# Kernel optimization log

Measured on AMD Instinct MI355X. Metric: run time of the kernel, lower is better.

The kernel has to match this reference:

```python
import jax, jax.numpy as jnp
import numpy as np

N, T, S, H, HC, LMH = 100, 2, 6, 64, 64, 128  # zones, timesteps, state, actor/critic GRU hidden, localized hidden
MAX_ACTION = 3.0
NB = (S + 1) * 5  # 35: neighbor-concat feature size


def setup_inputs() -> dict:
    key = jax.random.key(0)
    ks = iter(jax.random.split(key, 40))
    def rn(shape, s=0.05):
        return jax.random.normal(next(ks), shape, dtype=jnp.float32) * s
    B = 2048
    return {
        "x": jax.random.normal(next(ks), (B, T, N, S), dtype=jnp.float32),
        # 100 independent SubActor parameter sets, stacked along leading unit axis
        "a_Wih": rn((N, 3 * H, S)), "a_Whh": rn((N, 3 * H, H)),
        "a_bih": rn((N, 3 * H)), "a_bhh": rn((N, 3 * H)),
        "a_W1": rn((N, H, H)), "a_b1": rn((N, H)),
        "a_W2": rn((N, H, H)), "a_b2": rn((N, H)),
        "a_W3": rn((N, 1, H)), "a_b3": rn((N, 1)),
        # LocalizedModule 99 (only index 99 survives the buggy critic loop)
        "lm_W1": rn((LMH, NB)), "lm_b1": rn((LMH,)),
        "lm_W2": rn((LMH, LMH)), "lm_b2": rn((LMH,)),
        "lm_W3": rn((1, LMH)), "lm_b3": rn((1,)),
        # SubCritic 99
        "sc_Wih": rn((3 * HC, NB)), "sc_Whh": rn((3 * HC, HC)),
        "sc_bih": rn((3 * HC,)), "sc_bhh": rn((3 * HC,)),
        "sc_W1": rn((HC, HC)), "sc_b1": rn((HC,)),
        "sc_W2": rn((HC, HC)), "sc_b2": rn((HC,)),
        "sc_W3": rn((1, HC)), "sc_b3": rn((1,)),
    }


def _gru_cell(gx, gh, h):
    # PyTorch GRU gate order: r, z, n
    xr, xz, xn = jnp.split(gx, 3, axis=-1)
    hr, hz, hn = jnp.split(gh, 3, axis=-1)
    r = jax.nn.sigmoid(xr + hr)
    z = jax.nn.sigmoid(xz + hz)
    n = jnp.tanh(xn + r * hn)
    return (1.0 - z) * n + z * h


def _forward(x, a_Wih, a_Whh, a_bih, a_bhh, a_W1, a_b1, a_W2, a_b2, a_W3, a_b3,
             lm_W1, lm_b1, lm_W2, lm_b2, lm_W3, lm_b3,
             sc_Wih, sc_Whh, sc_bih, sc_bhh, sc_W1, sc_b1, sc_W2, sc_b2, sc_W3, sc_b3):
    B = x.shape[0]
    # ---- ActorNetwork: 100 independent GRU+MLP units, batched over unit axis n ----
    gx = jnp.einsum('btns,ngs->btng', x, a_Wih) + a_bih  # [B,T,N,3H]
    def astep(h, gx_t):
        gh = jnp.einsum('bnh,ngh->bng', h, a_Whh) + a_bhh
        h2 = _gru_cell(gx_t, gh, h)
        return h2, h2
    h0 = jnp.zeros((B, N, H), x.dtype)
    _, hs = jax.lax.scan(astep, h0, jnp.moveaxis(gx, 1, 0))
    hseq = jnp.moveaxis(hs, 0, 1)  # [B,T,N,H]
    a = jax.nn.relu(hseq)
    a = jax.nn.relu(jnp.einsum('btnh,nkh->btnk', a, a_W1) + a_b1)
    a = jax.nn.relu(jnp.einsum('btnh,nkh->btnk', a, a_W2) + a_b2)
    a = MAX_ACTION * (jax.nn.sigmoid(jnp.einsum('btnh,nkh->btnk', a, a_W3) + a_b3) - 0.5)  # [B,T,N,1]
    # torch.stack over units -> (N,B,T,1), then .view(-1,T,N): subactor-major flat reinterpretation
    p = jnp.transpose(a[..., 0], (2, 0, 1)).reshape(B, T, N)
    xc = jnp.concatenate([x, p[..., None]], axis=-1)  # [B,T,N,S+1]
    # ---- CriticNetwork: f/q lists are reset inside the loop, so only i=99 contributes ----
    # neighbors of 99: (99, 89, 100->zeros, 109->zeros, 98)
    z7 = jnp.zeros_like(xc[:, :, 99])
    xi = jnp.concatenate([xc[:, :, 99], xc[:, :, 89], z7, z7, xc[:, :, 98]], axis=-1)  # [B,T,35]
    # LocalizedModule 99 on last timestep
    f = jax.nn.relu(xi[:, -1] @ lm_W1.T + lm_b1)
    f = jax.nn.relu(f @ lm_W2.T + lm_b2)
    f = f @ lm_W3.T + lm_b3  # [B,1]
    # SubCritic 99: GRU then per-timestep MLP; only last timestep is returned,
    # and the MLP is per-timestep, so applying it to the last hidden state is exact.
    cgx = xi @ sc_Wih.T + sc_bih  # [B,T,3HC]
    def cstep(h, gx_t):
        gh = h @ sc_Whh.T + sc_bhh
        h2 = _gru_cell(gx_t, gh, h)
        return h2, h2
    h_last, _ = jax.lax.scan(cstep, jnp.zeros((B, HC), x.dtype), jnp.moveaxis(cgx, 1, 0))
    c = jax.nn.relu(h_last)
    c = jax.nn.relu(c @ sc_W1.T + sc_b1)
    c = jax.nn.relu(c @ sc_W2.T + sc_b2)
    q = c @ sc_W3.T + sc_b3  # [B,1]
    q_total = jnp.sum(f + q, axis=1)  # [B]
    return p[:, -1], q_total.reshape(-1, 1)


def reference(x, a_Wih, a_Whh, a_bih, a_bhh, a_W1, a_b1, a_W2, a_b2, a_W3, a_b3,
              lm_W1, lm_b1, lm_W2, lm_b2, lm_W3, lm_b3,
              sc_Wih, sc_Whh, sc_bih, sc_bhh, sc_W1, sc_b1, sc_W2, sc_b2, sc_W3, sc_b3):
    return _forward(x, a_Wih, a_Whh, a_bih, a_bhh, a_W1, a_b1, a_W2, a_b2, a_W3, a_b3,
                    lm_W1, lm_b1, lm_W2, lm_b2, lm_W3, lm_b3,
                    sc_Wih, sc_Whh, sc_bih, sc_bhh, sc_W1, sc_b1, sc_W2, sc_b2, sc_W3, sc_b3)
```

## Files before the change

kernel.cpp:

```cpp
#include <hip/hip_runtime.h>
#include <hip/hip_bf16.h>

typedef __attribute__((ext_vector_type(8))) short short8;
typedef __attribute__((ext_vector_type(4))) float f32x4;

#define SLAB 44032
#define WS_W_OFF 1638400
#define WS_CW_OFF (WS_W_OFF + 100 * SLAB)
#define E_SLAB 1100800
#define E_CW   48064

#define OFF_X 44032
#define OFF_H 48128
#define OFF_A 64512
#define LDS_TOTAL 80896

__device__ __forceinline__ unsigned pkbf(float a, float b) {
    __hip_bfloat162 h = __float22bfloat162_rn(make_float2(a, b));
    return *reinterpret_cast<unsigned*>(&h);
}
__device__ __forceinline__ float sigf(float x) {
    return __builtin_amdgcn_rcpf(1.f + __builtin_amdgcn_exp2f(-1.4426950408889634f * x));
}
__device__ __forceinline__ float tanhfast(float y) {
    return 1.f - 2.f * __builtin_amdgcn_rcpf(1.f + __builtin_amdgcn_exp2f(2.8853900817779268f * y));
}
__device__ __forceinline__ void g2l16(const void* g, void* l) {
    __builtin_amdgcn_global_load_lds(
        (const __attribute__((address_space(1))) void*)g,
        (__attribute__((address_space(3))) void*)l, 16, 0, 0);
}

__global__ __launch_bounds__(256)
void convert_kernel(const float* __restrict__ Wih, const float* __restrict__ Whh,
                    const float* __restrict__ W1, const float* __restrict__ W2,
                    const float* __restrict__ scWih, const float* __restrict__ scWhh,
                    const float* __restrict__ scW1, const float* __restrict__ scW2,
                    const float* __restrict__ lmW1, const float* __restrict__ lmW2,
                    char* __restrict__ slab, float* __restrict__ cw)
{
    int idx = blockIdx.x * 256 + threadIdx.x;
    if (idx < E_SLAB) {
        int n = idx / 11008;
        int i = idx - n * 11008;
        char* zs = slab + (size_t)n * SLAB;
        if (i < 768) {
            int row = i >> 2, j = i & 3;
            const float* g = Wih + n * 1152 + row * 6;
            float a = (2 * j < 6) ? g[2 * j] : 0.f;
            float b = (2 * j + 1 < 6) ? g[2 * j + 1] : 0.f;
            *(unsigned*)(zs + row * 16 + j * 4) = pkbf(a, b);
        } else if (i < 6912) {
            int k = i - 768, row = k >> 5, j = k & 31;
            float2 v = *(const float2*)(Whh + n * 12288 + row * 64 + j * 2);
            *(unsigned*)(zs + 3072 + row * 128 + ((j * 4) ^ ((row & 7) << 4))) = pkbf(v.x, v.y);
        } else if (i < 8960) {
            int k = i - 6912, row = k >> 5, j = k & 31;
            float2 v = *(const float2*)(W1 + n * 4096 + row * 64 + j * 2);
            *(unsigned*)(zs + 27648 + row * 128 + ((j * 4) ^ ((row & 7) << 4))) = pkbf(v.x, v.y);
        } else {
            int k = i - 8960, row = k >> 5, j = k & 31;
            float2 v = *(const float2*)(W2 + n * 4096 + row * 64 + j * 2);
            *(unsigned*)(zs + 35840 + row * 128 + ((j * 4) ^ ((row & 7) << 4))) = pkbf(v.x, v.y);
        }
        return;
    }
    int i = idx - E_SLAB;
    if (i >= E_CW) return;
    float v;
    if (i < 6720)        { int c = i / 192,          j = i - c * 192;          v = scWih[j * 35 + c]; }
    else if (i < 19008)  { int k = (i - 6720) / 192, j = (i - 6720) - k * 192; v = scWhh[j * 64 + k]; }
    else if (i < 23104)  { int k = (i - 19008) / 64, j = (i - 19008) - k * 64; v = scW1[j * 64 + k]; }
    else if (i < 27200)  { int k = (i - 23104) / 64, j = (i - 23104) - k * 64; v = scW2[j * 64 + k]; }
    else if (i < 31680)  { int c = (i - 27200) / 128, j = (i - 27200) - c * 128; v = lmW1[j * 35 + c]; }
    else                 { int k = (i - 31680) / 128, j = (i - 31680) - k * 128; v = lmW2[j * 128 + k]; }
    cw[i] = v;
}

__global__ __launch_bounds__(256, 2)
void actor_kernel(const float* __restrict__ x, const char* __restrict__ slab,
                  const float* __restrict__ bih, const float* __restrict__ bhh,
                  const float* __restrict__ b1, const float* __restrict__ b2,
                  const float* __restrict__ W3, const float* __restrict__ b3,
                  float* __restrict__ p_flat)
{
    extern __shared__ char sm[];
    const int tid   = threadIdx.x;
    const int n     = blockIdx.x >> 4;
    const int chunk = blockIdx.x & 15;
    const int w     = tid >> 6;
    const int l     = tid & 63;
    const int bcol  = l & 15;
    const int grp   = l >> 4;
    const int a7    = bcol & 7;
    const int ch0   = grp * 4;

    {
        const char* gz = slab + (size_t)n * SLAB;
        for (int i = w; i < 43; i += 4)
            g2l16(gz + i * 1024 + l * 16, sm + i * 1024);
        int t = tid >> 7, b = tid & 127;
        const float* xr = x + (size_t)(chunk * 128 + b) * 1200 + t * 600 + n * 6;
        uint4 pk;
        pk.x = pkbf(xr[0], xr[1]);
        pk.y = pkbf(xr[2], xr[3]);
        pk.z = pkbf(xr[4], xr[5]);
        pk.w = 0u;
        *(uint4*)(sm + OFF_X + (t * 128 + b) * 16) = pk;
    }
    __syncthreads();

    const int gsz = (grp ^ a7) << 4;
    const char* wihp = sm + bcol * 16;
    const char* whhA = sm + 3072  + bcol * 128 + gsz;
    const char* whhB = sm + 3072  + bcol * 128 + (gsz ^ 64);
    const char* w1A  = sm + 27648 + bcol * 128 + gsz;
    const char* w1B  = sm + 27648 + bcol * 128 + (gsz ^ 64);
    const char* w2A  = sm + 35840 + bcol * 128 + gsz;
    const char* w2B  = sm + 35840 + bcol * 128 + (gsz ^ 64);
    char* hTile = sm + OFF_H + w * 4096;
    char* aTile = sm + OFF_A + w * 4096;
    const int wgr = (grp & 1) * 8;
    const int g1v = grp >> 1;

    const float* bihz = bih + n * 192;
    const float* bhhz = bhh + n * 192;
    f32x4 bRi[4], bZi[4], bXNi[4], bHNi[4];
#pragma unroll
    for (int mt = 0; mt < 4; ++mt) {
        const int ch = mt * 16 + ch0;
        bRi[mt]  = *(const f32x4*)&bihz[ch]      + *(const f32x4*)&bhhz[ch];
        bZi[mt]  = *(const f32x4*)&bihz[64 + ch] + *(const f32x4*)&bhhz[64 + ch];
        bXNi[mt] = *(const f32x4*)&bihz[128 + ch];
        bHNi[mt] = *(const f32x4*)&bhhz[128 + ch];
    }
    const float b3v = b3[n];
    const short8 zfrag = {0, 0, 0, 0, 0, 0, 0, 0};

    f32x4 hp[2][4];
#pragma unroll
    for (int nt = 0; nt < 2; ++nt)
#pragma unroll
        for (int mt = 0; mt < 4; ++mt) hp[nt][mt] = (f32x4){0.f, 0.f, 0.f, 0.f};

    for (int t = 0; t < 2; ++t) {
        short8 bxv[2] = {zfrag, zfrag};
        if (grp == 0) {
            bxv[0] = *(const short8*)(sm + OFF_X + (t * 128 + w * 32 + bcol) * 16);
            bxv[1] = *(const short8*)(sm + OFF_X + (t * 128 + w * 32 + 16 + bcol) * 16);
        }
        short8 bh0v[2], bh1v[2];
        if (t == 1) {
#pragma unroll
            for (int nt = 0; nt < 2; ++nt) {
                bh0v[nt] = *(const short8*)(hTile + (nt * 16 + bcol) * 128 + gsz);
                bh1v[nt] = *(const short8*)(hTile + (nt * 16 + bcol) * 128 + (gsz ^ 64));
            }
        }
#pragma unroll
        for (int mt = 0; mt < 4; ++mt) {
            f32x4 aR[2], aZ[2], aXN[2], aHN[2];
#pragma unroll
            for (int nt = 0; nt < 2; ++nt) {
                aR[nt] = bRi[mt]; aZ[nt] = bZi[mt]; aXN[nt] = bXNi[mt]; aHN[nt] = bHNi[mt];
            }
            short8 wr = zfrag, wzg = zfrag, wn = zfrag;
            if (grp == 0) {
                wr  = *(const short8*)(wihp + (0 + mt) * 256);
                wzg = *(const short8*)(wihp + (4 + mt) * 256);
                wn  = *(const short8*)(wihp + (8 + mt) * 256);
            }
#pragma unroll
            for (int nt = 0; nt < 2; ++nt) {
                aR[nt]  = __builtin_amdgcn_mfma_f32_16x16x32_bf16(wr,  bxv[nt], aR[nt],  0, 0, 0);
                aZ[nt]  = __builtin_amdgcn_mfma_f32_16x16x32_bf16(wzg, bxv[nt], aZ[nt],  0, 0, 0);
                aXN[nt] = __builtin_amdgcn_mfma_f32_16x16x32_bf16(wn,  bxv[nt], aXN[nt], 0, 0, 0);
            }
            if (t == 1) {
                short8 r0 = *(const short8*)(whhA + (0 + mt) * 2048);
                short8 r1 = *(const short8*)(whhB + (0 + mt) * 2048);
                short8 z0 = *(const short8*)(whhA + (4 + mt) * 2048);
                short8 z1 = *(const short8*)(whhB + (4 + mt) * 2048);
                short8 n0 = *(const short8*)(whhA + (8 + mt) * 2048);
                short8 n1 = *(const short8*)(whhB + (8 + mt) * 2048);
#pragma unroll
                for (int nt = 0; nt < 2; ++nt) {
                    aR[nt]  = __builtin_amdgcn_mfma_f32_16x16x32_bf16(r0, bh0v[nt], aR[nt],  0, 0, 0);
                    aR[nt]  = __builtin_amdgcn_mfma_f32_16x16x32_bf16(r1, bh1v[nt], aR[nt],  0, 0, 0);
                    aZ[nt]  = __builtin_amdgcn_mfma_f32_16x16x32_bf16(z0, bh0v[nt], aZ[nt],  0, 0, 0);
                    aZ[nt]  = __builtin_amdgcn_mfma_f32_16x16x32_bf16(z1, bh1v[nt], aZ[nt],  0, 0, 0);
                    aHN[nt] = __builtin_amdgcn_mfma_f32_16x16x32_bf16(n0, bh0v[nt], aHN[nt], 0, 0, 0);
                    aHN[nt] = __builtin_amdgcn_mfma_f32_16x16x32_bf16(n1, bh1v[nt], aHN[nt], 0, 0, 0);
                }
            }
#pragma unroll
            for (int nt = 0; nt < 2; ++nt) {
                f32x4 h2;
#pragma unroll
                for (int r = 0; r < 4; ++r) {
                    float rg = sigf(aR[nt][r]);
                    float zg = sigf(aZ[nt][r]);
                    float nn = tanhfast(aXN[nt][r] + rg * aHN[nt][r]);
                    h2[r] = nn + zg * (hp[nt][mt][r] - nn);
                }
                hp[nt][mt] = h2;
                char* wmt = hTile + nt * 2048 + bcol * 128 + wgr + (((2 * mt + g1v) ^ a7) << 4);
                if (t == 0) {
                    uint2 ph; ph.x = pkbf(h2[0], h2[1]); ph.y = pkbf(h2[2], h2[3]);
                    *(uint2*)wmt = ph;
                }
                uint2 pa;
                pa.x = pkbf(fmaxf(h2[0], 0.f), fmaxf(h2[1], 0.f));
                pa.y = pkbf(fmaxf(h2[2], 0.f), fmaxf(h2[3], 0.f));
                *(uint2*)(wmt + 16384) = pa;
            }
        }
        {
            short8 ba0[2], ba1[2];
#pragma unroll
            for (int nt = 0; nt < 2; ++nt) {
                ba0[nt] = *(const short8*)(aTile + (nt * 16 + bcol) * 128 + gsz);
                ba1[nt] = *(const short8*)(aTile + (nt * 16 + bcol) * 128 + (gsz ^ 64));
            }
#pragma unroll
            for (int mt = 0; mt < 4; ++mt) {
                short8 wa  = *(const short8*)(w1A + mt * 2048);
                short8 wbv = *(const short8*)(w1B + mt * 2048);
                f32x4 bmv = *(const f32x4*)&b1[n * 64 + mt * 16 + ch0];
#pragma unroll
                for (int nt = 0; nt < 2; ++nt) {
                    f32x4 m1 = bmv;
                    m1 = __builtin_amdgcn_mfma_f32_16x16x32_bf16(wa,  ba0[nt], m1, 0, 0, 0);
                    m1 = __builtin_amdgcn_mfma_f32_16x16x32_bf16(wbv, ba1[nt], m1, 0, 0, 0);
                    uint2 pm;
                    pm.x = pkbf(fmaxf(m1[0], 0.f), fmaxf(m1[1], 0.f));
                    pm.y = pkbf(fmaxf(m1[2], 0.f), fmaxf(m1[3], 0.f));
                    *(uint2*)(aTile + nt * 2048 + bcol * 128 + wgr + (((2 * mt + g1v) ^ a7) << 4)) = pm;
                }
            }
        }
        {
            short8 bm0[2], bm1[2];
#pragma unroll
            for (int nt = 0; nt < 2; ++nt) {
                bm0[nt] = *(const short8*)(aTile + (nt * 16 + bcol) * 128 + gsz);
                bm1[nt] = *(const short8*)(aTile + (nt * 16 + bcol) * 128 + (gsz ^ 64));
            }
            float part[2] = {0.f, 0.f};
#pragma unroll
            for (int mt = 0; mt < 4; ++mt) {
                short8 wa  = *(const short8*)(w2A + mt * 2048);
                short8 wbv = *(const short8*)(w2B + mt * 2048);
                f32x4 bmv = *(const f32x4*)&b2[n * 64 + mt * 16 + ch0];
                f32x4 w3v = *(const f32x4*)&W3[n * 64 + mt * 16 + ch0];
#pragma unroll
                for (int nt = 0; nt < 2; ++nt) {
                    f32x4 m2 = bmv;
                    m2 = __builtin_amdgcn_mfma_f32_16x16x32_bf16(wa,  bm0[nt], m2, 0, 0, 0);
                    m2 = __builtin_amdgcn_mfma_f32_16x16x32_bf16(wbv, bm1[nt], m2, 0, 0, 0);
#pragma unroll
                    for (int r = 0; r < 4; ++r)
                        part[nt] += w3v[r] * fmaxf(m2[r], 0.f);
                }
            }
#pragma unroll
            for (int nt = 0; nt < 2; ++nt) {
                part[nt] += __shfl_xor(part[nt], 16, 64);
                part[nt] += __shfl_xor(part[nt], 32, 64);
            }
            if (l < 16) {
#pragma unroll
                for (int nt = 0; nt < 2; ++nt) {
                    int bg = chunk * 128 + w * 32 + nt * 16 + bcol;
                    float val = 3.f * (sigf(part[nt] + b3v) - 0.5f);
                    p_flat[n * 4096 + bg * 2 + t] = val;
                }
            }
        }
    }
}

__global__ __launch_bounds__(256, 2)
void critic_kernel(const float* __restrict__ x, const float* __restrict__ p_flat,
                   const float* __restrict__ cw,
                   const float* __restrict__ lmb1, const float* __restrict__ lmb2,
                   const float* __restrict__ lmW3, const float* __restrict__ lmb3,
                   const float* __restrict__ scbih, const float* __restrict__ scbhh,
                   const float* __restrict__ scb1, const float* __restrict__ scb2,
                   const float* __restrict__ scW3, const float* __restrict__ scb3,
                   float* __restrict__ out)
{
    const float* tWih = cw;
    const float* tWhh = cw + 6720;
    const float* tW1  = cw + 19008;
    const float* tW2  = cw + 23104;
    const float* tlm1 = cw + 27200;
    const float* tlm2 = cw + 31680;

    __shared__ float sxi[4][72];
    __shared__ float shh[4][68];
    __shared__ float sab[4][68];
    __shared__ float sc1[4][68];
    __shared__ float sf1[4][132];

    const int tid = threadIdx.x;
    const int wid = tid >> 6;
    const int lane = tid & 63;
    const int b = blockIdx.x * 4 + wid;

    for (int idx = lane; idx < 72; idx += 64) {
        int t = idx / 36, c = idx - t * 36;
        float v = 0.f;
        if (c < 35) {
            int g = c / 7, e = c - g * 7;
            int z = (g == 0) ? 99 : (g == 1) ? 89 : (g == 4) ? 98 : -1;
            if (z >= 0)
                v = (e < 6) ? x[((size_t)b * 2 + t) * 600 + z * 6 + e]
                            : p_flat[b * 200 + t * 100 + z];
        }
        sxi[wid][idx] = v;
    }
    __syncthreads();

    float cg00 = scbih[lane], cg01 = scbih[lane + 64], cg02 = scbih[lane + 128];
    float cg10 = cg00, cg11 = cg01, cg12 = cg02;
#pragma unroll 5
    for (int c = 0; c < 35; ++c) {
        float w0 = tWih[c * 192 + lane];
        float w1 = tWih[c * 192 + 64 + lane];
        float w2 = tWih[c * 192 + 128 + lane];
        float x0 = sxi[wid][c], x1 = sxi[wid][36 + c];
        cg00 += w0 * x0; cg01 += w1 * x0; cg02 += w2 * x0;
        cg10 += w0 * x1; cg11 += w1 * x1; cg12 += w2 * x1;
    }
    const float bhr = scbhh[lane], bhz = scbhh[lane + 64], bhn = scbhh[lane + 128];
    float r  = 1.f / (1.f + expf(-(cg00 + bhr)));
    float zg = 1.f / (1.f + expf(-(cg01 + bhz)));
    float nn = tanhf(cg02 + r * bhn);
    float hj = (1.f - zg) * nn;
    shh[wid][lane] = hj;
    __syncthreads();
    float ghr = bhr, ghz = bhz, ghn = bhn;
#pragma unroll 8
    for (int k = 0; k < 64; ++k) {
        float hk = shh[wid][k];
        ghr += tWhh[k * 192 + lane] * hk;
        ghz += tWhh[k * 192 + 64 + lane] * hk;
        ghn += tWhh[k * 192 + 128 + lane] * hk;
    }
    r  = 1.f / (1.f + expf(-(cg10 + ghr)));
    zg = 1.f / (1.f + expf(-(cg11 + ghz)));
    nn = tanhf(cg12 + r * ghn);
    hj = (1.f - zg) * nn + zg * hj;
    sab[wid][lane] = fmaxf(hj, 0.f);
    __syncthreads();
    float acc = scb1[lane];
#pragma unroll 8
    for (int k = 0; k < 64; ++k)
        acc += tW1[k * 64 + lane] * sab[wid][k];
    sc1[wid][lane] = fmaxf(acc, 0.f);
    __syncthreads();
    float acc2 = scb2[lane];
#pragma unroll 8
    for (int k = 0; k < 64; ++k)
        acc2 += tW2[k * 64 + lane] * sc1[wid][k];
    float qpart = scW3[lane] * fmaxf(acc2, 0.f);
    float f1a = lmb1[lane], f1c = lmb1[lane + 64];
#pragma unroll 5
    for (int c = 0; c < 35; ++c) {
        float xv = sxi[wid][36 + c];
        f1a += tlm1[c * 128 + lane] * xv;
        f1c += tlm1[c * 128 + 64 + lane] * xv;
    }
    sf1[wid][lane] = fmaxf(f1a, 0.f);
    sf1[wid][lane + 64] = fmaxf(f1c, 0.f);
    __syncthreads();
    float f2a = lmb2[lane], f2c = lmb2[lane + 64];
#pragma unroll 8
    for (int k = 0; k < 128; ++k) {
        float fv = sf1[wid][k];
        f2a += tlm2[k * 128 + lane] * fv;
        f2c += tlm2[k * 128 + 64 + lane] * fv;
    }
    float fpart = lmW3[lane] * fmaxf(f2a, 0.f) + lmW3[lane + 64] * fmaxf(f2c, 0.f);

    float tot = qpart + fpart;
    for (int m = 32; m > 0; m >>= 1) tot += __shfl_xor(tot, m, 64);
    if (lane == 0) out[204800 + b] = tot + scb3[0] + lmb3[0];

    for (int l2 = lane; l2 < 100; l2 += 64)
        out[b * 100 + l2] = p_flat[b * 200 + 100 + l2];
}

extern "C" void kernel_launch(void* const* d_in, const int* in_sizes, int n_in,
                              void* d_out, int out_size, void* d_ws, size_t ws_size,
                              hipStream_t stream) {
    const float* x     = (const float*)d_in[0];
    const float* aWih  = (const float*)d_in[1];
    const float* aWhh  = (const float*)d_in[2];
    const float* abih  = (const float*)d_in[3];
    const float* abhh  = (const float*)d_in[4];
    const float* aW1   = (const float*)d_in[5];
    const float* ab1   = (const float*)d_in[6];
    const float* aW2   = (const float*)d_in[7];
    const float* ab2   = (const float*)d_in[8];
    const float* aW3   = (const float*)d_in[9];
    const float* ab3   = (const float*)d_in[10];
    const float* lmW1  = (const float*)d_in[11];
    const float* lmb1  = (const float*)d_in[12];
    const float* lmW2  = (const float*)d_in[13];
    const float* lmb2  = (const float*)d_in[14];
    const float* lmW3  = (const float*)d_in[15];
    const float* lmb3  = (const float*)d_in[16];
    const float* scWih = (const float*)d_in[17];
    const float* scWhh = (const float*)d_in[18];
    const float* scbih = (const float*)d_in[19];
    const float* scbhh = (const float*)d_in[20];
    const float* scW1  = (const float*)d_in[21];
    const float* scb1  = (const float*)d_in[22];
    const float* scW2  = (const float*)d_in[23];
    const float* scb2  = (const float*)d_in[24];
    const float* scW3  = (const float*)d_in[25];
    const float* scb3  = (const float*)d_in[26];
    float* out = (float*)d_out;
    float* p_flat = (float*)d_ws;
    char* slab = (char*)d_ws + WS_W_OFF;
    float* cw  = (float*)((char*)d_ws + WS_CW_OFF);

    hipFuncSetAttribute((const void*)actor_kernel,
                        hipFuncAttributeMaxDynamicSharedMemorySize, LDS_TOTAL);

    convert_kernel<<<dim3((E_SLAB + E_CW + 255) / 256), 256, 0, stream>>>(
        aWih, aWhh, aW1, aW2, scWih, scWhh, scW1, scW2, lmW1, lmW2, slab, cw);

    actor_kernel<<<dim3(1600), 256, LDS_TOTAL, stream>>>(
        x, slab, abih, abhh, ab1, ab2, aW3, ab3, p_flat);

    critic_kernel<<<dim3(512), 256, 0, stream>>>(
        x, p_flat, cw, lmb1, lmb2, lmW3, lmb3,
        scbih, scbhh, scb1, scb2, scW3, scb3, out);
}
```

Measured before the change: 78.20 us.

## Process two batch sub-chunks per actor block to amortize weight slab loads

The actor grid is halved so each block handles 256 batch rows in two sequential sub-chunks. The per-unit weight slab is staged into LDS once and reused for both, halving total global-to-LDS weight traffic. The second sub-chunk's inputs are prefetched into registers up front. MFMA sections are wrapped in s_setprio raises, and the per-warp x tile layout is reworked. Fewer blocks (800 on a large GPU) may reduce parallelism and latency hiding.

```diff
diff --git a/kernel.cpp b/kernel.cpp
--- a/kernel.cpp
+++ b/kernel.cpp
@@ -86,27 +86,37 @@
 {
     extern __shared__ char sm[];
     const int tid   = threadIdx.x;
-    const int n     = blockIdx.x >> 4;
-    const int chunk = blockIdx.x & 15;
+    const int n     = blockIdx.x >> 3;
+    const int bigc  = blockIdx.x & 7;
     const int w     = tid >> 6;
     const int l     = tid & 63;
     const int bcol  = l & 15;
     const int grp   = l >> 4;
     const int a7    = bcol & 7;
     const int ch0   = grp * 4;
-
+    char* uXw = sm + OFF_X + w * 1024;
+
+    float f1x0, f1x1, f1x2, f1x3, f1x4, f1x5;
     {
         const char* gz = slab + (size_t)n * SLAB;
         for (int i = w; i < 43; i += 4)
             g2l16(gz + i * 1024 + l * 16, sm + i * 1024);
-        int t = tid >> 7, b = tid & 127;
-        const float* xr = x + (size_t)(chunk * 128 + b) * 1200 + t * 600 + n * 6;
+        int tt = l >> 5, bb = l & 31;
+        const float* xr0 = x + (size_t)(bigc * 256 + w * 32 + bb) * 1200 + tt * 600 + n * 6;
+        const float* xr1 = xr0 + 128 * 1200;
+        float2 a0 = *(const float2*)xr0;
+        float2 a1 = *(const float2*)(xr0 + 2);
+        float2 a2 = *(const float2*)(xr0 + 4);
+        float2 c0 = *(const float2*)xr1;
+        float2 c1 = *(const float2*)(xr1 + 2);
+        float2 c2 = *(const float2*)(xr1 + 4);
+        f1x0 = c0.x; f1x1 = c0.y; f1x2 = c1.x; f1x3 = c1.y; f1x4 = c2.x; f1x5 = c2.y;
         uint4 pk;
-        pk.x = pkbf(xr[0], xr[1]);
-        pk.y = pkbf(xr[2], xr[3]);
-        pk.z = pkbf(xr[4], xr[5]);
+        pk.x = pkbf(a0.x, a0.y);
+        pk.y = pkbf(a1.x, a1.y);
+        pk.z = pkbf(a2.x, a2.y);
         pk.w = 0u;
-        *(uint4*)(sm + OFF_X + (t * 128 + b) * 16) = pk;
+        *(uint4*)(uXw + (tt * 32 + bb) * 16) = pk;
     }
     __syncthreads();
 
@@ -137,143 +147,169 @@
     const float b3v = b3[n];
     const short8 zfrag = {0, 0, 0, 0, 0, 0, 0, 0};
 
-    f32x4 hp[2][4];
-#pragma unroll
-    for (int nt = 0; nt < 2; ++nt)
-#pragma unroll
-        for (int mt = 0; mt < 4; ++mt) hp[nt][mt] = (f32x4){0.f, 0.f, 0.f, 0.f};
-
-    for (int t = 0; t < 2; ++t) {
-        short8 bxv[2] = {zfrag, zfrag};
-        if (grp == 0) {
-            bxv[0] = *(const short8*)(sm + OFF_X + (t * 128 + w * 32 + bcol) * 16);
-            bxv[1] = *(const short8*)(sm + OFF_X + (t * 128 + w * 32 + 16 + bcol) * 16);
+    for (int sc = 0; sc < 2; ++sc) {
+        if (sc == 1) {
+            int tt = l >> 5, bb = l & 31;
+            uint4 pk;
+            pk.x = pkbf(f1x0, f1x1);
+            pk.y = pkbf(f1x2, f1x3);
+            pk.z = pkbf(f1x4, f1x5);
+            pk.w = 0u;
+            *(uint4*)(uXw + (tt * 32 + bb) * 16) = pk;
         }
-        short8 bh0v[2], bh1v[2];
-        if (t == 1) {
-#pragma unroll
-            for (int nt = 0; nt < 2; ++nt) {
-                bh0v[nt] = *(const short8*)(hTile + (nt * 16 + bcol) * 128 + gsz);
-                bh1v[nt] = *(const short8*)(hTile + (nt * 16 + bcol) * 128 + (gsz ^ 64));
+        f32x4 hp[2][4];
+#pragma unroll
+        for (int nt = 0; nt < 2; ++nt)
+#pragma unroll
+            for (int mt = 0; mt < 4; ++mt) hp[nt][mt] = (f32x4){0.f, 0.f, 0.f, 0.f};
+
+        for (int t = 0; t < 2; ++t) {
+            short8 bxv[2] = {zfrag, zfrag};
+            if (grp == 0) {
+                bxv[0] = *(const short8*)(uXw + (t * 32 + bcol) * 16);
+                bxv[1] = *(const short8*)(uXw + (t * 32 + 16 + bcol) * 16);
             }
-        }
-#pragma unroll
-        for (int mt = 0; mt < 4; ++mt) {
-            f32x4 aR[2], aZ[2], aXN[2], aHN[2];
-#pragma unroll
-            for (int nt = 0; nt < 2; ++nt) {
-                aR[nt] = bRi[mt]; aZ[nt] = bZi[mt]; aXN[nt] = bXNi[mt]; aHN[nt] = bHNi[mt];
+            short8 bh0v[2], bh1v[2];
+            if (t == 1) {
+#pragma unroll
+                for (int nt = 0; nt < 2; ++nt) {
+                    bh0v[nt] = *(const short8*)(hTile + (nt * 16 + bcol) * 128 + gsz);
+                    bh1v[nt] = *(const short8*)(hTile + (nt * 16 + bcol) * 128 + (gsz ^ 64));
+                }
             }
-            short8 wr = zfrag, wzg = zfrag, wn = zfrag;
-            if (grp == 0) {
-                wr  = *(const short8*)(wihp + (0 + mt) * 256);
-                wzg = *(const short8*)(wihp + (4 + mt) * 256);
-                wn  = *(const short8*)(wihp + (8 + mt) * 256);
+#pragma unroll
+            for (int mt = 0; mt < 4; ++mt) {
+                f32x4 aR[2], aZ[2], aXN[2], aHN[2];
+#pragma unroll
+                for (int nt = 0; nt < 2; ++nt) {
+                    aR[nt] = bRi[mt]; aZ[nt] = bZi[mt]; aXN[nt] = bXNi[mt]; aHN[nt] = bHNi[mt];
+                }
+                short8 wr = zfrag, wzg = zfrag, wn = zfrag;
+                if (grp == 0) {
+                    wr  = *(const short8*)(wihp + (0 + mt) * 256);
+                    wzg = *(const short8*)(wihp + (4 + mt) * 256);
+                    wn  = *(const short8*)(wihp + (8 + mt) * 256);
+                }
+                __builtin_amdgcn_s_setprio(1);
+#pragma unroll
+                for (int nt = 0; nt < 2; ++nt) {
+                    aR[nt]  = __builtin_amdgcn_mfma_f32_16x16x32_bf16(wr,  bxv[nt], aR[nt],  0, 0, 0);
+                    aZ[nt]  = __builtin_amdgcn_mfma_f32_16x16x32_bf16(wzg, bxv[nt], aZ[nt],  0, 0, 0);
+                    aXN[nt] = __builtin_amdgcn_mfma_f32_16x16x32_bf16(wn,  bxv[nt], aXN[nt], 0, 0, 0);
+                }
+                if (t == 1) {
+                    short8 r0 = *(const short8*)(whhA + (0 + mt) * 2048);
+                    short8 r1 = *(const short8*)(whhB + (0 + mt) * 2048);
+                    short8 z0 = *(const short8*)(whhA + (4 + mt) * 2048);
+                    short8 z1 = *(const short8*)(whhB + (4 + mt) * 2048);
+                    short8 n0 = *(const short8*)(whhA + (8 + mt) * 2048);
+                    short8 n1 = *(const short8*)(whhB + (8 + mt) * 2048);
+#pragma unroll
+                    for (int nt = 0; nt < 2; ++nt) {
+                        aR[nt]  = __builtin_amdgcn_mfma_f32_16x16x32_bf16(r0, bh0v[nt], aR[nt],  0, 0, 0);
+                        aR[nt]  = __builtin_amdgcn_mfma_f32_16x16x32_bf16(r1, bh1v[nt], aR[nt],  0, 0, 0);
+                        aZ[nt]  = __builtin_amdgcn_mfma_f32_16x16x32_bf16(z0, bh0v[nt], aZ[nt],  0, 0, 0);
+                        aZ[nt]  = __builtin_amdgcn_mfma_f32_16x16x32_bf16(z1, bh1v[nt], aZ[nt],  0, 0, 0);
+                        aHN[nt] = __builtin_amdgcn_mfma_f32_16x16x32_bf16(n0, bh0v[nt], aHN[nt], 0, 0, 0);
+                        aHN[nt] = __builtin_amdgcn_mfma_f32_16x16x32_bf16(n1, bh1v[nt], aHN[nt], 0, 0, 0);
+                    }
+                }
+                __builtin_amdgcn_s_setprio(0);
+#pragma unroll
+                for (int nt = 0; nt < 2; ++nt) {
+                    f32x4 h2;
+#pragma unroll
+                    for (int r = 0; r < 4; ++r) {
+                        float rg = sigf(aR[nt][r]);
+                        float zg = sigf(aZ[nt][r]);
+                        float nn = tanhfast(aXN[nt][r] + rg * aHN[nt][r]);
+                        h2[r] = nn + zg * (hp[nt][mt][r] - nn);
+                    }
+                    hp[nt][mt] = h2;
+                    char* wmt = hTile + nt * 2048 + bcol * 128 + wgr + (((2 * mt + g1v) ^ a7) << 4);
+                    if (t == 0) {
+                        uint2 ph; ph.x = pkbf(h2[0], h2[1]); ph.y = pkbf(h2[2], h2[3]);
+                        *(uint2*)wmt = ph;
+                    }
+                    uint2 pa;
+                    pa.x = pkbf(fmaxf(h2[0], 0.f), fmaxf(h2[1], 0.f));
+                    pa.y = pkbf(fmaxf(h2[2], 0.f), fmaxf(h2[3], 0.f));
+                    *(uint2*)(wmt + 16384) = pa;
+                }
             }
-#pragma unroll
-            for (int nt = 0; nt < 2; ++nt) {
-                aR[nt]  = __builtin_amdgcn_mfma_f32_16x16x32_bf16(wr,  bxv[nt], aR[nt],  0, 0, 0);
-                aZ[nt]  = __builtin_amdgcn_mfma_f32_16x16x32_bf16(wzg, bxv[nt], aZ[nt],  0, 0, 0);
-                aXN[nt] = __builtin_amdgcn_mfma_f32_16x16x32_bf16(wn,  bxv[nt], aXN[nt], 0, 0, 0);
+            {
+                short8 ba0[2], ba1[2];
+#pragma unroll
+                for (int nt = 0; nt < 2; ++nt) {
+                    ba0[nt] = *(const short8*)(aTile + (nt * 16 + bcol) * 128 + gsz);
+                    ba1[nt] = *(const short8*)(aTile + (nt * 16 + bcol) * 128 + (gsz ^ 64));
+                }
+#pragma unroll
+                for (int mt = 0; mt < 4; ++mt) {
+                    short8 wa  = *(const short8*)(w1A + mt * 2048);
+                    short8 wbv = *(const short8*)(w1B + mt * 2048);
+                    f32x4 bmv = *(const f32x4*)&b1[n * 64 + mt * 16 + ch0];
+                    __builtin_amdgcn_s_setprio(1);
+                    f32x4 m1o[2];
+#pragma unroll
+                    for (int nt = 0; nt < 2; ++nt) {
+                        f32x4 m1 = bmv;
+                        m1 = __builtin_amdgcn_mfma_f32_16x16x32_bf16(wa,  ba0[nt], m1, 0, 0, 0);
+                        m1 = __builtin_amdgcn_mfma_f32_16x16x32_bf16(wbv, ba1[nt], m1, 0, 0, 0);
+                        m1o[nt] = m1;
+                    }
+                    __builtin_amdgcn_s_setprio(0);
+#pragma unroll
+                    for (int nt = 0; nt < 2; ++nt) {
+                        uint2 pm;
+                        pm.x = pkbf(fmaxf(m1o[nt][0], 0.f), fmaxf(m1o[nt][1], 0.f));
+                        pm.y = pkbf(fmaxf(m1o[nt][2], 0.f), fmaxf(m1o[nt][3], 0.f));
+                        *(uint2*)(aTile + nt * 2048 + bcol * 128 + wgr + (((2 * mt + g1v) ^ a7) << 4)) = pm;
+                    }
+                }
             }
-            if (t == 1) {
-                short8 r0 = *(const short8*)(whhA + (0 + mt) * 2048);
-                short8 r1 = *(const short8*)(whhB + (0 + mt) * 2048);
-                short8 z0 = *(const short8*)(whhA + (4 + mt) * 2048);
-                short8 z1 = *(const short8*)(whhB + (4 + mt) * 2048);
-                short8 n0 = *(const short8*)(whhA + (8 + mt) * 2048);
-                short8 n1 = *(const short8*)(whhB + (8 + mt) * 2048);
-#pragma unroll
-                for (int nt = 0; nt < 2; ++nt) {
-                    aR[nt]  = __builtin_amdgcn_mfma_f32_16x16x32_bf16(r0, bh0v[nt], aR[nt],  0, 0, 0);
-                    aR[nt]  = __builtin_amdgcn_mfma_f32_16x16x32_bf16(r1, bh1v[nt], aR[nt],  0, 0, 0);
-                    aZ[nt]  = __builtin_amdgcn_mfma_f32_16x16x32_bf16(z0, bh0v[nt], aZ[nt],  0, 0, 0);
-                    aZ[nt]  = __builtin_amdgcn_mfma_f32_16x16x32_bf16(z1, bh1v[nt], aZ[nt],  0, 0, 0);
-                    aHN[nt] = __builtin_amdgcn_mfma_f32_16x16x32_bf16(n0, bh0v[nt], aHN[nt], 0, 0, 0);
-                    aHN[nt] = __builtin_amdgcn_mfma_f32_16x16x32_bf16(n1, bh1v[nt], aHN[nt], 0, 0, 0);
-                }
-            }
-#pragma unroll
-            for (int nt = 0; nt < 2; ++nt) {
-                f32x4 h2;
-#pragma unroll
-                for (int r = 0; r < 4; ++r) {
-                    float rg = sigf(aR[nt][r]);
-                    float zg = sigf(aZ[nt][r]);
-                    float nn = tanhfast(aXN[nt][r] + rg * aHN[nt][r]);
-                    h2[r] = nn + zg * (hp[nt][mt][r] - nn);
-                }
-                hp[nt][mt] = h2;
-                char* wmt = hTile + nt * 2048 + bcol * 128 + wgr + (((2 * mt + g1v) ^ a7) << 4);
-                if (t == 0) {
-                    uint2 ph; ph.x = pkbf(h2[0], h2[1]); ph.y = pkbf(h2[2], h2[3]);
-                    *(uint2*)wmt = ph;
-                }
-                uint2 pa;
-                pa.x = pkbf(fmaxf(h2[0], 0.f), fmaxf(h2[1], 0.f));
-                pa.y = pkbf(fmaxf(h2[2], 0.f), fmaxf(h2[3], 0.f));
-                *(uint2*)(wmt + 16384) = pa;
-            }
-        }
-        {
-            short8 ba0[2], ba1[2];
-#pragma unroll
-            for (int nt = 0; nt < 2; ++nt) {
-                ba0[nt] = *(const short8*)(aTile + (nt * 16 + bcol) * 128 + gsz);
-                ba1[nt] = *(const short8*)(aTile + (nt * 16 + bcol) * 128 + (gsz ^ 64));
-            }
-#pragma unroll
-            for (int mt = 0; mt < 4; ++mt) {
-                short8 wa  = *(const short8*)(w1A + mt * 2048);
-                short8 wbv = *(const short8*)(w1B + mt * 2048);
-                f32x4 bmv = *(const f32x4*)&b1[n * 64 + mt * 16 + ch0];
-#pragma unroll
-                for (int nt = 0; nt < 2; ++nt) {
-                    f32x4 m1 = bmv;
-                    m1 = __builtin_amdgcn_mfma_f32_16x16x32_bf16(wa,  ba0[nt], m1, 0, 0, 0);
-                    m1 = __builtin_amdgcn_mfma_f32_16x16x32_bf16(wbv, ba1[nt], m1, 0, 0, 0);
-                    uint2 pm;
-                    pm.x = pkbf(fmaxf(m1[0], 0.f), fmaxf(m1[1], 0.f));
-                    pm.y = pkbf(fmaxf(m1[2], 0.f), fmaxf(m1[3], 0.f));
-                    *(uint2*)(aTile + nt * 2048 + bcol * 128 + wgr + (((2 * mt + g1v) ^ a7) << 4)) = pm;
-                }
-            }
-        }
-        {
-            short8 bm0[2], bm1[2];
-#pragma unroll
-            for (int nt = 0; nt < 2; ++nt) {
-                bm0[nt] = *(const short8*)(aTile + (nt * 16 + bcol) * 128 + gsz);
-                bm1[nt] = *(const short8*)(aTile + (nt * 16 + bcol) * 128 + (gsz ^ 64));
-            }
-            float part[2] = {0.f, 0.f};
-#pragma unroll
-            for (int mt = 0; mt < 4; ++mt) {
-                short8 wa  = *(const short8*)(w2A + mt * 2048);
-                short8 wbv = *(const short8*)(w2B + mt * 2048);
-                f32x4 bmv = *(const f32x4*)&b2[n * 64 + mt * 16 + ch0];
-                f32x4 w3v = *(const f32x4*)&W3[n * 64 + mt * 16 + ch0];
-#pragma unroll
-                for (int nt = 0; nt < 2; ++nt) {
-                    f32x4 m2 = bmv;
-                    m2 = __builtin_amdgcn_mfma_f32_16x16x32_bf16(wa,  bm0[nt], m2, 0, 0, 0);
-                    m2 = __builtin_amdgcn_mfma_f32_16x16x32_bf16(wbv, bm1[nt], m2, 0, 0, 0);
-#pragma unroll
-                    for (int r = 0; r < 4; ++r)
-                        part[nt] += w3v[r] * fmaxf(m2[r], 0.f);
-                }
-            }
-#pragma unroll
-            for (int nt = 0; nt < 2; ++nt) {
-                part[nt] += __shfl_xor(part[nt], 16, 64);
-                part[nt] += __shfl_xor(part[nt], 32, 64);
-            }
-            if (l < 16) {
-#pragma unroll
-                for (int nt = 0; nt < 2; ++nt) {
-                    int bg = chunk * 128 + w * 32 + nt * 16 + bcol;
-                    float val = 3.f * (sigf(part[nt] + b3v) - 0.5f);
-                    p_flat[n * 4096 + bg * 2 + t] = val;
+            {
+                short8 bm0[2], bm1[2];
+#pragma unroll
+                for (int nt = 0; nt < 2; ++nt) {
+                    bm0[nt] = *(const short8*)(aTile + (nt * 16 + bcol) * 128 + gsz);
+                    bm1[nt] = *(const short8*)(aTile + (nt * 16 + bcol) * 128 + (gsz ^ 64));
+                }
+                float part[2] = {0.f, 0.f};
+#pragma unroll
+                for (int mt = 0; mt < 4; ++mt) {
+                    short8 wa  = *(const short8*)(w2A + mt * 2048);
+                    short8 wbv = *(const short8*)(w2B + mt * 2048);
+                    f32x4 bmv = *(const f32x4*)&b2[n * 64 + mt * 16 + ch0];
+                    f32x4 w3v = *(const f32x4*)&W3[n * 64 + mt * 16 + ch0];
+                    __builtin_amdgcn_s_setprio(1);
+                    f32x4 m2o[2];
+#pragma unroll
+                    for (int nt = 0; nt < 2; ++nt) {
+                        f32x4 m2 = bmv;
+                        m2 = __builtin_amdgcn_mfma_f32_16x16x32_bf16(wa,  bm0[nt], m2, 0, 0, 0);
+                        m2 = __builtin_amdgcn_mfma_f32_16x16x32_bf16(wbv, bm1[nt], m2, 0, 0, 0);
+                        m2o[nt] = m2;
+                    }
+                    __builtin_amdgcn_s_setprio(0);
+#pragma unroll
+                    for (int nt = 0; nt < 2; ++nt)
+#pragma unroll
+                        for (int r = 0; r < 4; ++r)
+                            part[nt] += w3v[r] * fmaxf(m2o[nt][r], 0.f);
+                }
+#pragma unroll
+                for (int nt = 0; nt < 2; ++nt) {
+                    part[nt] += __shfl_xor(part[nt], 16, 64);
+                    part[nt] += __shfl_xor(part[nt], 32, 64);
+                }
+                if (l < 16) {
+#pragma unroll
+                    for (int nt = 0; nt < 2; ++nt) {
+                        int bg = bigc * 256 + sc * 128 + w * 32 + nt * 16 + bcol;
+                        float val = 3.f * (sigf(part[nt] + b3v) - 0.5f);
+                        p_flat[n * 4096 + bg * 2 + t] = val;
+                    }
                 }
             }
         }
@@ -433,7 +469,7 @@
     convert_kernel<<<dim3((E_SLAB + E_CW + 255) / 256), 256, 0, stream>>>(
         aWih, aWhh, aW1, aW2, scWih, scWhh, scW1, scW2, lmW1, lmW2, slab, cw);
 
-    actor_kernel<<<dim3(1600), 256, LDS_TOTAL, stream>>>(
+    actor_kernel<<<dim3(800), 256, LDS_TOTAL, stream>>>(
         x, slab, abih, abhh, ab1, ab2, aW3, ab3, p_flat);
 
     critic_kernel<<<dim3(512), 256, 0, stream>>>(
```

After: 83.45 us. +6.7%, slower.
